# Kernel tuning notes

Hardware: AMD Instinct MI355X
Metric: run time of the kernel (lower is better)

## Reference

```python
import jax, jax.numpy as jnp
import numpy as np

NUM_OPS = 100_000
NUM_MACH = 512
H = 128
OPF = 6
MF = 2
L = 2
N_PREC = 800_000
N_CHALF = 800_000  # compat edges per direction
EPS = 1e-5


def setup_inputs() -> dict:
    key = jax.random.key(0)
    ks = jax.random.split(key, 20)
    op_features = jax.random.normal(ks[0], (NUM_OPS, OPF), dtype=jnp.float32)
    machine_features = jax.random.normal(ks[1], (NUM_MACH, MF), dtype=jnp.float32)
    prec_src = jax.random.randint(ks[2], (N_PREC,), 0, NUM_OPS, dtype=jnp.int32)
    prec_tgt = jax.random.randint(ks[3], (N_PREC,), 0, NUM_OPS, dtype=jnp.int32)
    precedence_edges = jnp.stack([prec_src, prec_tgt])  # [2, N_PREC]
    op_idx = jax.random.randint(ks[4], (N_CHALF,), 0, NUM_OPS, dtype=jnp.int32)
    m_idx = jax.random.randint(ks[5], (N_CHALF,), 0, NUM_MACH, dtype=jnp.int32)
    # bidirectional pairs in unified node space (machines offset by NUM_OPS)
    src = jnp.concatenate([op_idx, m_idx + NUM_OPS])
    tgt = jnp.concatenate([m_idx + NUM_OPS, op_idx])
    compatibility_edges = jnp.stack([src, tgt])  # [2, 2*N_CHALF]
    s = 0.05
    op_emb_W = jax.random.normal(ks[6], (H, OPF), dtype=jnp.float32) * s
    op_emb_b = jnp.zeros((H,), jnp.float32)
    mach_emb_W = jax.random.normal(ks[7], (H, MF), dtype=jnp.float32) * s
    mach_emb_b = jnp.zeros((H,), jnp.float32)
    prec_W = jax.random.normal(ks[8], (L, H, H), dtype=jnp.float32) * s
    prec_b = jax.random.normal(ks[9], (L, H), dtype=jnp.float32) * s
    compat_W = jax.random.normal(ks[10], (L, H, H), dtype=jnp.float32) * s
    compat_b = jax.random.normal(ks[11], (L, H), dtype=jnp.float32) * s
    op_ln_g = jnp.ones((L, H), jnp.float32)
    op_ln_b = jnp.zeros((L, H), jnp.float32)
    mach_ln_g = jnp.ones((L, H), jnp.float32)
    mach_ln_b = jnp.zeros((L, H), jnp.float32)
    return dict(op_features=op_features, machine_features=machine_features,
                precedence_edges=precedence_edges, compatibility_edges=compatibility_edges,
                op_emb_W=op_emb_W, op_emb_b=op_emb_b, mach_emb_W=mach_emb_W, mach_emb_b=mach_emb_b,
                prec_W=prec_W, prec_b=prec_b, compat_W=compat_W, compat_b=compat_b,
                op_ln_g=op_ln_g, op_ln_b=op_ln_b, mach_ln_g=mach_ln_g, mach_ln_b=mach_ln_b)


def _layer_norm(x, g, b):
    mu = jnp.mean(x, axis=-1, keepdims=True)
    var = jnp.mean(jnp.square(x - mu), axis=-1, keepdims=True)
    return (x - mu) * jax.lax.rsqrt(var + EPS) * g + b


def _scatter_mean(vals, idx, mask, n):
    # vals [E,H], idx [E], mask [E] bool (or None); mean over incoming edges, count clamped >= 1
    if mask is not None:
        vals = jnp.where(mask[:, None], vals, 0.0)
        idx = jnp.where(mask, idx, 0)
        ones = mask.astype(vals.dtype)
    else:
        ones = jnp.ones(idx.shape, vals.dtype)
    sums = jax.ops.segment_sum(vals, idx, num_segments=n)
    cnts = jax.ops.segment_sum(ones, idx, num_segments=n)
    return sums / jnp.maximum(cnts, 1.0)[:, None]


def _forward(op_features, machine_features, precedence_edges, compatibility_edges,
             op_emb_W, op_emb_b, mach_emb_W, mach_emb_b,
             prec_W, prec_b, compat_W, compat_b,
             op_ln_g, op_ln_b, mach_ln_g, mach_ln_b):
    num_ops = op_features.shape[0]
    num_mach = machine_features.shape[0]
    op_emb = op_features @ op_emb_W.T + op_emb_b
    mach_emb = machine_features @ mach_emb_W.T + mach_emb_b

    p_src, p_tgt = precedence_edges[0], precedence_edges[1]
    c_src, c_tgt = compatibility_edges[0], compatibility_edges[1]
    op2m = (c_src < num_ops) & (c_tgt >= num_ops)
    m2o = (c_src >= num_ops) & (c_tgt < num_ops)
    o2m_src = jnp.where(op2m, c_src, 0)
    o2m_tgt = jnp.where(op2m, c_tgt - num_ops, 0)
    m2o_src = jnp.where(m2o, c_src - num_ops, 0)
    m2o_tgt = jnp.where(m2o, c_tgt, 0)

    for l in range(L):
        # precedence (op -> op): linear-then-gather == gather-then-linear
        op_t = op_emb @ prec_W[l].T + prec_b[l]            # [num_ops, H]
        op_emb_prec = _scatter_mean(op_t[p_src], p_tgt, None, num_ops)
        # compatibility, shared linear for both directions
        op_c = op_emb @ compat_W[l].T + compat_b[l]        # [num_ops, H]
        mach_c = mach_emb @ compat_W[l].T + compat_b[l]    # [num_mach, H]
        mach_emb_compat = _scatter_mean(op_c[o2m_src], o2m_tgt, op2m, num_mach)
        op_emb_compat = _scatter_mean(mach_c[m2o_src], m2o_tgt, m2o, num_ops)
        op_emb = _layer_norm(op_emb + op_emb_prec + op_emb_compat, op_ln_g[l], op_ln_b[l])
        mach_emb = _layer_norm(mach_emb + mach_emb_compat, mach_ln_g[l], mach_ln_b[l])
    return op_emb, mach_emb


def reference(op_features, machine_features, precedence_edges, compatibility_edges,
              op_emb_W, op_emb_b, mach_emb_W, mach_emb_b,
              prec_W, prec_b, compat_W, compat_b,
              op_ln_g, op_ln_b, mach_ln_g, mach_ln_b):
    return _forward(op_features, machine_features, precedence_edges, compatibility_edges,
                    op_emb_W, op_emb_b, mach_emb_W, mach_emb_b,
                    prec_W, prec_b, compat_W, compat_b,
                    op_ln_g, op_ln_b, mach_ln_g, mach_ln_b)
```

## Files before the change

### kernel.cpp

```cpp
#include <hip/hip_runtime.h>
#include <hip/hip_bf16.h>

#define NUM_OPS   100000
#define NUM_MACH  512
#define HDIM      128
#define P1        100352
#define NHIST     200704
#define NBLK      196
#define NCOARSE   784
#define NBC       256
#define NBM       256
#define MHWORDS   (NUM_MACH * NBM)
#define NBLK_M    128
#define NBLK_T    (NBLK + NBLK_M)

typedef short short8 __attribute__((ext_vector_type(8)));
typedef unsigned short ushort8 __attribute__((ext_vector_type(8)));
typedef float floatx4 __attribute__((ext_vector_type(4)));

__device__ __forceinline__ unsigned short f2bf(float f) {
    unsigned u = __float_as_uint(f);
    unsigned r = (u + 0x7FFFu + ((u >> 16) & 1u)) >> 16;
    return (unsigned short)r;
}
__device__ __forceinline__ float bf2f(unsigned short u) {
    return __uint_as_float(((unsigned)u) << 16);
}

__global__ void k_prep(const float* __restrict__ Fo, const float* __restrict__ Fm,
                       const float* __restrict__ Wo, const float* __restrict__ bo,
                       const float* __restrict__ Wm, const float* __restrict__ bm,
                       const float* __restrict__ Wp, const float* __restrict__ Wc,
                       unsigned short* __restrict__ op_ebf,
                       float* __restrict__ mach_emb, unsigned short* __restrict__ mach_ebf,
                       unsigned short* __restrict__ Wb) {
    int idx = blockIdx.x * blockDim.x + threadIdx.x;
    if (idx < NUM_OPS * HDIM) {
        int r = idx >> 7, h = idx & 127;
        const float* f = Fo + (size_t)r * 6;
        const float* w = Wo + (size_t)h * 6;
        float s = bo[h];
#pragma unroll
        for (int i = 0; i < 6; ++i) s += f[i] * w[i];
        op_ebf[idx] = f2bf(s);
        return;
    }
    idx -= NUM_OPS * HDIM;
    if (idx < NUM_MACH * HDIM) {
        int r = idx >> 7, h = idx & 127;
        const float* f = Fm + (size_t)r * 2;
        const float* w = Wm + (size_t)h * 2;
        float s = bm[h] + f[0] * w[0] + f[1] * w[1];
        mach_emb[idx] = s;
        mach_ebf[idx] = f2bf(s);
        return;
    }
    idx -= NUM_MACH * HDIM;
    if (idx < 2 * 128 * 256) {
        int l = idx >> 15, h = (idx >> 8) & 127, k = idx & 255;
        float v = (k < 128) ? Wp[(size_t)l * 16384 + h * 128 + k]
                            : Wc[(size_t)l * 16384 + h * 128 + (k - 128)];
        Wb[idx] = f2bf(v);
    }
}

__global__ __launch_bounds__(256) void k_front(const int* __restrict__ prec_e, int nprec,
                                               const int* __restrict__ comp_e, int E, int M,
                                               int* __restrict__ chist_bh,
                                               int* __restrict__ mach_bh) {
    __shared__ int hc[NCOARSE];
    __shared__ int hm[NUM_MACH];
    for (int i = threadIdx.x; i < NCOARSE; i += 256) hc[i] = 0;
    for (int i = threadIdx.x; i < NUM_MACH; i += 256) hm[i] = 0;
    __syncthreads();
    int NT = nprec + E;
    int ch = (NT + NBC - 1) / NBC;
    int i0 = blockIdx.x * ch, i1 = min(NT, i0 + ch);
    for (int i = i0 + threadIdx.x; i < i1; i += 256) {
        int key;
        if (i < nprec) key = prec_e[nprec + i];
        else {
            int e = i - nprec;
            key = P1 + comp_e[e];
            atomicAdd(&hm[comp_e[E + e] - M], 1);
        }
        atomicAdd(&hc[key >> 8], 1);
    }
    __syncthreads();
    for (int i = threadIdx.x; i < NCOARSE; i += 256)
        chist_bh[i * NBC + blockIdx.x] = hc[i];
    for (int i = threadIdx.x; i < NUM_MACH; i += 256)
        mach_bh[i * NBC + blockIdx.x] = hm[i];
}

__global__ __launch_bounds__(256) void k_cfill(const int* __restrict__ prec_e, int nprec,
                                               const int* __restrict__ comp_e, int E, int M,
                                               const int* __restrict__ scan,
                                               int* __restrict__ pairs) {
    __shared__ int cur[NCOARSE];
    for (int i = threadIdx.x; i < NCOARSE; i += 256) cur[i] = scan[i * NBC + blockIdx.x];
    __syncthreads();
    int NT = nprec + E;
    int ch = (NT + NBC - 1) / NBC;
    int i0 = blockIdx.x * ch, i1 = min(NT, i0 + ch);
    for (int i = i0 + threadIdx.x; i < i1; i += 256) {
        int key, val;
        if (i < nprec) { key = prec_e[nprec + i]; val = prec_e[i]; }
        else { int e = i - nprec; key = P1 + comp_e[e]; val = comp_e[E + e] - M; }
        int pos = atomicAdd(&cur[key >> 8], 1);
        pairs[pos] = (val << 8) | (key & 255);
    }
}

__global__ __launch_bounds__(256) void k_blocksum(const int* __restrict__ arr, int* __restrict__ partial) {
    __shared__ int sh[256];
    int b = blockIdx.x, t = threadIdx.x;
    int4 v = *(const int4*)(arr + b * 1024 + t * 4);
    sh[t] = v.x + v.y + v.z + v.w;
    __syncthreads();
    for (int o = 128; o; o >>= 1) { if (t < o) sh[t] += sh[t + o]; __syncthreads(); }
    if (!t) partial[b] = sh[0];
}

__global__ __launch_bounds__(256) void k_scanpart(const int* __restrict__ partial,
                                                  int* __restrict__ block_off) {
    __shared__ int sh[256];
    int t = threadIdx.x;
    int seg0 = blockIdx.x ? NBLK : 0;
    int n    = blockIdx.x ? NBLK_M : NBLK;
    int v = (t < n) ? partial[seg0 + t] : 0;
    sh[t] = v; __syncthreads();
    for (int o = 1; o < 256; o <<= 1) {
        int x = (t >= o) ? sh[t - o] : 0; __syncthreads();
        sh[t] += x; __syncthreads();
    }
    if (t < n) block_off[seg0 + t] = sh[t] - v;
}

__global__ __launch_bounds__(256) void k_scanwrite(const int* __restrict__ arr,
                                                   const int* __restrict__ block_off,
                                                   int* __restrict__ rs) {
    __shared__ int sh[256];
    int b = blockIdx.x, t = threadIdx.x;
    int base_i = b * 1024 + t * 4;
    int4 v = *(const int4*)(arr + base_i);
    int tsum = v.x + v.y + v.z + v.w;
    sh[t] = tsum; __syncthreads();
    for (int o = 1; o < 256; o <<= 1) {
        int x = (t >= o) ? sh[t - o] : 0; __syncthreads();
        sh[t] += x; __syncthreads();
    }
    int off = block_off[b] + sh[t] - tsum;
    int4 r; r.x = off; r.y = off + v.x; r.z = off + v.x + v.y; r.w = off + v.x + v.y + v.z;
    *(int4*)(rs + base_i) = r;
}

__global__ __launch_bounds__(256) void k_finefill(const int* __restrict__ scans, int NT,
                                                  const int* __restrict__ pairs,
                                                  int* __restrict__ rs,
                                                  int* __restrict__ bucket_all,
                                                  const int* __restrict__ comp_e, int E, int M,
                                                  int* __restrict__ bucket_mach,
                                                  int* __restrict__ mach_rs) {
    int t = threadIdx.x;
    if (blockIdx.x < NCOARSE) {
        __shared__ int hh[256];
        __shared__ int ex[256];
        __shared__ int cu[256];
        int b = blockIdx.x;
        int s = scans[b * NBC];
        int e = (b == NCOARSE - 1) ? NT : scans[(b + 1) * NBC];
        hh[t] = 0;
        __syncthreads();
        for (int i = s + t; i < e; i += 256) atomicAdd(&hh[pairs[i] & 255], 1);
        __syncthreads();
        int v = hh[t];
        ex[t] = v; __syncthreads();
        for (int o = 1; o < 256; o <<= 1) {
            int x = (t >= o) ? ex[t - o] : 0; __syncthreads();
            ex[t] += x; __syncthreads();
        }
        int start = s + ex[t] - v;
        rs[b * 256 + t] = start;
        cu[t] = start;
        __syncthreads();
        for (int i = s + t; i < e; i += 256) {
            int p = pairs[i];
            int pos = atomicAdd(&cu[p & 255], 1);
            bucket_all[pos] = ((unsigned)p) >> 8;
        }
    } else {
        __shared__ int cur[NUM_MACH];
        int blk = blockIdx.x - NCOARSE;
        const int* moff = scans + NHIST;
        for (int i = t; i < NUM_MACH; i += 256) cur[i] = moff[i * NBM + blk];
        if (blk == 0) {
            for (int m = t; m < NUM_MACH; m += 256) mach_rs[m] = moff[m * NBM];
            if (t == 0) mach_rs[NUM_MACH] = E;
        }
        __syncthreads();
        int nprec = NT - E;
        int chNT = (NT + NBC - 1) / NBC;
        int e0 = blk * chNT - nprec;       if (e0 < 0) e0 = 0;
        int e1 = (blk + 1) * chNT - nprec; if (e1 > E) e1 = E;
        for (int e = e0 + t; e < e1; e += 256) {
            int m = comp_e[E + e] - M;
            int op = comp_e[e];
            int pos = atomicAdd(&cur[m], 1);
            bucket_mach[pos] = op;
        }
    }
}

__device__ __forceinline__ void gather8(const unsigned short* __restrict__ src,
                                        const int* __restrict__ bucket,
                                        int s0, int e0, int start, int step,
                                        int lane, int g, int d, float* a) {
    for (int base = s0 + start; base < e0; base += step) {
        int cnt = min(64, e0 - base);
        int idx = (lane < cnt) ? bucket[base + lane] : 0;
        for (int j = 0; j < cnt; j += 4) {
            int jj = j + g;
            int rowi = __shfl(idx, jj);
            short8 v = *(const short8*)(src + (size_t)rowi * HDIM + d);
            if (jj < cnt) {
#pragma unroll
                for (int k = 0; k < 8; ++k) a[k] += bf2f((unsigned short)v[k]);
            }
        }
    }
}

__global__ __launch_bounds__(256) void k_aggmg(
    const unsigned short* __restrict__ op_ebf, const unsigned short* __restrict__ mach_ebf,
    const int* __restrict__ rs, const int* __restrict__ bucket_all,
    unsigned short* __restrict__ Ab, int* __restrict__ flags, int M,
    const int* __restrict__ mach_rs, const int* __restrict__ bucket_mach,
    float* __restrict__ mach_sum, int nb_agg) {
    int wave = threadIdx.x >> 6, lane = threadIdx.x & 63;
    int g = lane >> 4;
    int d = (lane & 15) * 8;

    if ((int)blockIdx.x < nb_agg) {
        int r = blockIdx.x * 4 + wave;
        if (r >= M) return;

        float a[8];
#pragma unroll
        for (int k = 0; k < 8; ++k) a[k] = 0.f;
        int s0 = rs[r], e0 = rs[r + 1];
        gather8(op_ebf, bucket_all, s0, e0, 0, 64, lane, g, d, a);
#pragma unroll
        for (int k = 0; k < 8; ++k) {
            a[k] += __shfl_xor(a[k], 16);
            a[k] += __shfl_xor(a[k], 32);
        }
        float pinv = 1.f / fmaxf((float)(e0 - s0), 1.f);

        float b[8];
#pragma unroll
        for (int k = 0; k < 8; ++k) b[k] = 0.f;
        int s1 = rs[P1 + r], e1 = rs[P1 + r + 1];
        gather8(mach_ebf, bucket_all, s1, e1, 0, 64, lane, g, d, b);
#pragma unroll
        for (int k = 0; k < 8; ++k) {
            b[k] += __shfl_xor(b[k], 16);
            b[k] += __shfl_xor(b[k], 32);
        }
        float cinv = 1.f / fmaxf((float)(e1 - s1), 1.f);

        if (lane < 16) {
            ushort8 pa, pb;
#pragma unroll
            for (int k = 0; k < 8; ++k) { pa[k] = f2bf(a[k] * pinv); pb[k] = f2bf(b[k] * cinv); }
            *(ushort8*)(Ab + (size_t)r * 256 + d)       = pa;
            *(ushort8*)(Ab + (size_t)r * 256 + 128 + d) = pb;
        }
        if (lane == 0) flags[r] = (e0 > s0 ? 1 : 0) | (e1 > s1 ? 2 : 0);
        return;
    }

    int b2 = blockIdx.x - nb_agg;
    int m  = b2 & 511;
    int yq = b2 >> 9;
    int s0 = mach_rs[m], e0 = mach_rs[m + 1];
    float a[8];
#pragma unroll
    for (int k = 0; k < 8; ++k) a[k] = 0.f;
    gather8(op_ebf, bucket_mach, s0, e0, (yq * 4 + wave) * 64, 1024, lane, g, d, a);
#pragma unroll
    for (int k = 0; k < 8; ++k) {
        a[k] += __shfl_xor(a[k], 16);
        a[k] += __shfl_xor(a[k], 32);
    }
    if (lane < 16) {
#pragma unroll
        for (int k = 0; k < 8; ++k)
            atomicAdd(&mach_sum[m * HDIM + d + k], a[k]);
    }
}

__global__ __launch_bounds__(256) void k_gemm_mfma(
    const unsigned short* __restrict__ Ab, const unsigned short* __restrict__ embb,
    const unsigned short* __restrict__ Wb,
    const float* __restrict__ bp, const float* __restrict__ bc,
    const int* __restrict__ flags,
    const float* __restrict__ g, const float* __restrict__ bt,
    float* __restrict__ dstf, unsigned short* __restrict__ dstb, int M) {
    int wave = threadIdx.x >> 6, lane = threadIdx.x & 63;
    int m0 = blockIdx.x * 64 + wave * 16;
    if (m0 >= M) return;
    int quad = lane >> 4, col = lane & 15;

    floatx4 acc[8];
#pragma unroll
    for (int t = 0; t < 8; ++t) acc[t] = (floatx4){0.f, 0.f, 0.f, 0.f};

    const short* Arow  = (const short*)(Ab + (size_t)(m0 + col) * 256);
    const short* Wbase = (const short*)Wb;

#pragma unroll
    for (int ks = 0; ks < 8; ++ks) {
        short8 a = *(const short8*)(Arow + ks * 32 + quad * 8);
#pragma unroll
        for (int t = 0; t < 8; ++t) {
            short8 b = *(const short8*)(Wbase + (size_t)(t * 16 + col) * 256 + ks * 32 + quad * 8);
            acc[t] = __builtin_amdgcn_mfma_f32_16x16x32_bf16(a, b, acc[t], 0, 0, 0);
        }
    }

    float bpv[8], bcv[8], gv[8], btv[8];
#pragma unroll
    for (int t = 0; t < 8; ++t) {
        int c = t * 16 + col;
        bpv[t] = bp[c]; bcv[t] = bc[c]; gv[t] = g[c]; btv[t] = bt[c];
    }
#pragma unroll
    for (int reg = 0; reg < 4; ++reg) {
        int r = m0 + quad * 4 + reg;
        int fl = flags[r];
        float fp = (fl & 1) ? 1.f : 0.f, fc = (fl & 2) ? 1.f : 0.f;
        float x[8]; float s = 0.f, q = 0.f;
#pragma unroll
        for (int t = 0; t < 8; ++t) {
            float v = acc[t][reg] + bf2f(embb[(size_t)r * HDIM + t * 16 + col]) + fp * bpv[t] + fc * bcv[t];
            x[t] = v; s += v; q += v * v;
        }
#pragma unroll
        for (int msk = 1; msk < 16; msk <<= 1) { s += __shfl_xor(s, msk); q += __shfl_xor(q, msk); }
        float mu = s * (1.f / 128.f);
        float rstd = rsqrtf(fmaxf(q * (1.f / 128.f) - mu * mu, 0.f) + 1e-5f);
#pragma unroll
        for (int t = 0; t < 8; ++t) {
            float y = (x[t] - mu) * rstd * gv[t] + btv[t];
            if (dstf) dstf[(size_t)r * HDIM + t * 16 + col] = y;
            if (dstb) dstb[(size_t)r * HDIM + t * 16 + col] = f2bf(y);
        }
    }
}

__global__ __launch_bounds__(128) void k_mach_update(
    const float* __restrict__ mach_emb, const float* __restrict__ mach_sum,
    const int* __restrict__ mach_rs,
    const float* __restrict__ Wc, const float* __restrict__ bc,
    const float* __restrict__ g, const float* __restrict__ bt,
    float* __restrict__ dst, unsigned short* __restrict__ dstb) {
    __shared__ float row[HDIM];
    __shared__ float red[4];
    int m = blockIdx.x, t = threadIdx.x;
    int cnt = mach_rs[m + 1] - mach_rs[m];
    float sc = (cnt > 0) ? 1.f / (float)cnt : 0.f;
    row[t] = mach_sum[m * HDIM + t] * sc;
    __syncthreads();
    float dot = bc[t];
    const float* w = Wc + (size_t)t * HDIM;
#pragma unroll 8
    for (int k = 0; k < HDIM; ++k) dot += row[k] * w[k];
    float x = mach_emb[m * HDIM + t] + ((cnt > 0) ? dot : 0.f);
    float s = x, q = x * x;
#pragma unroll
    for (int o = 32; o; o >>= 1) { s += __shfl_xor(s, o); q += __shfl_xor(q, o); }
    int wv = t >> 6;
    if ((t & 63) == 0) { red[wv * 2] = s; red[wv * 2 + 1] = q; }
    __syncthreads();
    s = red[0] + red[2]; q = red[1] + red[3];
    float mu = s * (1.f / 128.f);
    float rstd = rsqrtf(fmaxf(q * (1.f / 128.f) - mu * mu, 0.f) + 1e-5f);
    float y = (x - mu) * rstd * g[t] + bt[t];
    dst[m * HDIM + t] = y;
    if (dstb) dstb[m * HDIM + t] = f2bf(y);
}

extern "C" void kernel_launch(void* const* d_in, const int* in_sizes, int n_in,
                              void* d_out, int out_size, void* d_ws, size_t ws_size,
                              hipStream_t stream) {
    const float* op_feat    = (const float*)d_in[0];
    const float* m_feat     = (const float*)d_in[1];
    const int*   prec_e     = (const int*)d_in[2];
    const int*   comp_e     = (const int*)d_in[3];
    const float* op_emb_W   = (const float*)d_in[4];
    const float* op_emb_b   = (const float*)d_in[5];
    const float* mach_emb_W = (const float*)d_in[6];
    const float* mach_emb_b = (const float*)d_in[7];
    const float* prec_W     = (const float*)d_in[8];
    const float* prec_b     = (const float*)d_in[9];
    const float* compat_W   = (const float*)d_in[10];
    const float* compat_b   = (const float*)d_in[11];
    const float* op_ln_g    = (const float*)d_in[12];
    const float* op_ln_b    = (const float*)d_in[13];
    const float* mach_ln_g  = (const float*)d_in[14];
    const float* mach_ln_b  = (const float*)d_in[15];
    float* out = (float*)d_out;

    const int M = NUM_OPS, NM = NUM_MACH;
    const int nprec = in_sizes[2] / 2;
    const int ncomp = in_sizes[3] / 2;
    const int E = ncomp / 2;
    const int NT = nprec + E;

    float* ws = (float*)d_ws;
    size_t o = 0;
    unsigned short* op_ebf = (unsigned short*)(ws + o); o += (size_t)M * 64;
    unsigned short* Ab = (unsigned short*)(ws + o); o += (size_t)M * 128;
    unsigned short* Wb = (unsigned short*)(ws + o); o += 32768;
    float* mach_emb = ws + o; o += (size_t)NM * HDIM;
    unsigned short* mach_ebf = (unsigned short*)(ws + o); o += (size_t)NM * 64;
    float* mach_sum = ws + o; o += (size_t)NM * HDIM;
    int* ip = (int*)(ws + o);
    size_t io = 0;
    int* hists     = ip + io; io += NHIST + MHWORDS;
    int* scans     = ip + io; io += NHIST + MHWORDS;
    int* rs        = ip + io; io += NHIST;
    int* mach_rs   = ip + io; io += NM + 8;
    int* partialT  = ip + io; io += 512;
    int* block_off = ip + io; io += 512;
    int* flags     = ip + io; io += M;
    int* pairs     = ip + io; io += (size_t)NT;
    int* bucket_all  = ip + io; io += (size_t)NT;
    int* bucket_mach = ip + io; io += (size_t)E;

    int* mach_bh = hists + NHIST;

    k_front<<<NBC, 256, 0, stream>>>(prec_e, nprec, comp_e, E, M, hists, mach_bh);
    k_blocksum<<<NBLK_T, 256, 0, stream>>>(hists, partialT);
    k_scanpart<<<2, 256, 0, stream>>>(partialT, block_off);
    k_scanwrite<<<NBLK_T, 256, 0, stream>>>(hists, block_off, scans);
    k_cfill<<<NBC, 256, 0, stream>>>(prec_e, nprec, comp_e, E, M, scans, pairs);
    k_finefill<<<NCOARSE + NBM, 256, 0, stream>>>(scans, NT, pairs, rs, bucket_all,
                                                  comp_e, E, M, bucket_mach, mach_rs);

    int prep_total = (M + NM) * HDIM + 2 * 128 * 256;
    k_prep<<<(prep_total + 255) / 256, 256, 0, stream>>>(
        op_feat, m_feat, op_emb_W, op_emb_b, mach_emb_W, mach_emb_b,
        prec_W, compat_W, op_ebf, mach_emb, mach_ebf, Wb);

    const int nb_agg = (M + 3) / 4;
    for (int l = 0; l < 2; ++l) {
        int last = (l == 1);
        const float* bpl = prec_b   + (size_t)l * HDIM;
        const float* Wc  = compat_W + (size_t)l * HDIM * HDIM;
        const float* bcl = compat_b + (size_t)l * HDIM;

        hipMemsetAsync(mach_sum, 0, (size_t)NM * HDIM * sizeof(float), stream);

        k_aggmg<<<nb_agg + NM * 4, 256, 0, stream>>>(
            op_ebf, mach_ebf, rs, bucket_all, Ab, flags, M,
            mach_rs, bucket_mach, mach_sum, nb_agg);

        k_gemm_mfma<<<(M + 63) / 64, 256, 0, stream>>>(
            Ab, op_ebf, Wb + (size_t)l * 128 * 256, bpl, bcl, flags,
            op_ln_g + (size_t)l * HDIM, op_ln_b + (size_t)l * HDIM,
            last ? out : nullptr, last ? nullptr : op_ebf, M);

        k_mach_update<<<NM, 128, 0, stream>>>(
            mach_emb, mach_sum, mach_rs, Wc, bcl,
            mach_ln_g + (size_t)l * HDIM, mach_ln_b + (size_t)l * HDIM,
            last ? (out + (size_t)M * HDIM) : mach_emb, last ? nullptr : mach_ebf);
    }
}
```

Baseline: 567.0 us.

## Fuse neighbor aggregation with MFMA linear and layernorm in one kernel

Merges the gather/mean aggregation kernel and the MFMA GEMM+LayerNorm kernel into a single 1024-thread block kernel. Each block gathers 16 op rows into swizzled LDS and runs the 16x256x128 MFMA from LDS. It then applies bias and LayerNorm per row, so the intermediate Ab buffer and flags never go through global memory. Op embeddings are double-buffered (A/B) because the fused kernel reads neighbors of other rows while writing its own outputs, and machine aggregation is folded in as extra blocks with fewer waves per machine. The risk is lower occupancy from large blocks and barriers, and W is reloaded per block.

After: 561.3 us. About the same (-1.0%).

```diff
diff --git a/kernel.cpp b/kernel.cpp
--- a/kernel.cpp
+++ b/kernel.cpp
@@ -13,6 +13,7 @@
 #define MHWORDS   (NUM_MACH * NBM)
 #define NBLK_M    128
 #define NBLK_T    (NBLK + NBLK_M)
+#define NB_OP     (NUM_OPS / 16)
 
 typedef short short8 __attribute__((ext_vector_type(8)));
 typedef unsigned short ushort8 __attribute__((ext_vector_type(8)));
@@ -231,37 +232,61 @@
     }
 }
 
-__global__ __launch_bounds__(256) void k_aggmg(
-    const unsigned short* __restrict__ op_ebf, const unsigned short* __restrict__ mach_ebf,
+__global__ __launch_bounds__(1024, 8) void k_fused(
+    const unsigned short* __restrict__ ebf_src, const unsigned short* __restrict__ mach_ebf,
     const int* __restrict__ rs, const int* __restrict__ bucket_all,
-    unsigned short* __restrict__ Ab, int* __restrict__ flags, int M,
+    const unsigned short* __restrict__ Wb,
+    const float* __restrict__ bp, const float* __restrict__ bc,
+    const float* __restrict__ g, const float* __restrict__ bt,
+    float* __restrict__ dstf, unsigned short* __restrict__ dstb,
     const int* __restrict__ mach_rs, const int* __restrict__ bucket_mach,
-    float* __restrict__ mach_sum, int nb_agg) {
+    float* __restrict__ mach_sum, int M) {
+    __shared__ unsigned short At[16 * 256];
+    __shared__ float Xt[16][HDIM];
+    __shared__ int flg[16];
     int wave = threadIdx.x >> 6, lane = threadIdx.x & 63;
-    int g = lane >> 4;
-    int d = (lane & 15) * 8;
-
-    if ((int)blockIdx.x < nb_agg) {
-        int r = blockIdx.x * 4 + wave;
-        if (r >= M) return;
-
+    int gg = lane >> 4;
+    int d  = (lane & 15) * 8;
+
+    if ((int)blockIdx.x >= NB_OP) {
+        int m = blockIdx.x - NB_OP;
+        int s0 = mach_rs[m], e0 = mach_rs[m + 1];
         float a[8];
 #pragma unroll
         for (int k = 0; k < 8; ++k) a[k] = 0.f;
-        int s0 = rs[r], e0 = rs[r + 1];
-        gather8(op_ebf, bucket_all, s0, e0, 0, 64, lane, g, d, a);
+        gather8(ebf_src, bucket_mach, s0, e0, wave * 64, 1024, lane, gg, d, a);
 #pragma unroll
         for (int k = 0; k < 8; ++k) {
             a[k] += __shfl_xor(a[k], 16);
             a[k] += __shfl_xor(a[k], 32);
         }
+        if (lane < 16) {
+#pragma unroll
+            for (int k = 0; k < 8; ++k)
+                atomicAdd(&mach_sum[m * HDIM + d + k], a[k]);
+        }
+        return;
+    }
+
+    int r = blockIdx.x * 16 + wave;
+    {
+        float a[8];
+#pragma unroll
+        for (int k = 0; k < 8; ++k) a[k] = 0.f;
+        int s0 = rs[r], e0 = rs[r + 1];
+        gather8(ebf_src, bucket_all, s0, e0, 0, 64, lane, gg, d, a);
+#pragma unroll
+        for (int k = 0; k < 8; ++k) {
+            a[k] += __shfl_xor(a[k], 16);
+            a[k] += __shfl_xor(a[k], 32);
+        }
         float pinv = 1.f / fmaxf((float)(e0 - s0), 1.f);
 
         float b[8];
 #pragma unroll
         for (int k = 0; k < 8; ++k) b[k] = 0.f;
         int s1 = rs[P1 + r], e1 = rs[P1 + r + 1];
-        gather8(mach_ebf, bucket_all, s1, e1, 0, 64, lane, g, d, b);
+        gather8(mach_ebf, bucket_all, s1, e1, 0, 64, lane, gg, d, b);
 #pragma unroll
         for (int k = 0; k < 8; ++k) {
             b[k] += __shfl_xor(b[k], 16);
@@ -273,89 +298,53 @@
             ushort8 pa, pb;
 #pragma unroll
             for (int k = 0; k < 8; ++k) { pa[k] = f2bf(a[k] * pinv); pb[k] = f2bf(b[k] * cinv); }
-            *(ushort8*)(Ab + (size_t)r * 256 + d)       = pa;
-            *(ushort8*)(Ab + (size_t)r * 256 + 128 + d) = pb;
-        }
-        if (lane == 0) flags[r] = (e0 > s0 ? 1 : 0) | (e1 > s1 ? 2 : 0);
-        return;
-    }
-
-    int b2 = blockIdx.x - nb_agg;
-    int m  = b2 & 511;
-    int yq = b2 >> 9;
-    int s0 = mach_rs[m], e0 = mach_rs[m + 1];
-    float a[8];
-#pragma unroll
-    for (int k = 0; k < 8; ++k) a[k] = 0.f;
-    gather8(op_ebf, bucket_mach, s0, e0, (yq * 4 + wave) * 64, 1024, lane, g, d, a);
-#pragma unroll
-    for (int k = 0; k < 8; ++k) {
-        a[k] += __shfl_xor(a[k], 16);
-        a[k] += __shfl_xor(a[k], 32);
-    }
-    if (lane < 16) {
-#pragma unroll
-        for (int k = 0; k < 8; ++k)
-            atomicAdd(&mach_sum[m * HDIM + d + k], a[k]);
-    }
-}
-
-__global__ __launch_bounds__(256) void k_gemm_mfma(
-    const unsigned short* __restrict__ Ab, const unsigned short* __restrict__ embb,
-    const unsigned short* __restrict__ Wb,
-    const float* __restrict__ bp, const float* __restrict__ bc,
-    const int* __restrict__ flags,
-    const float* __restrict__ g, const float* __restrict__ bt,
-    float* __restrict__ dstf, unsigned short* __restrict__ dstb, int M) {
-    int wave = threadIdx.x >> 6, lane = threadIdx.x & 63;
-    int m0 = blockIdx.x * 64 + wave * 16;
-    if (m0 >= M) return;
-    int quad = lane >> 4, col = lane & 15;
-
-    floatx4 acc[8];
-#pragma unroll
-    for (int t = 0; t < 8; ++t) acc[t] = (floatx4){0.f, 0.f, 0.f, 0.f};
-
-    const short* Arow  = (const short*)(Ab + (size_t)(m0 + col) * 256);
-    const short* Wbase = (const short*)Wb;
-
-#pragma unroll
-    for (int ks = 0; ks < 8; ++ks) {
-        short8 a = *(const short8*)(Arow + ks * 32 + quad * 8);
-#pragma unroll
-        for (int t = 0; t < 8; ++t) {
-            short8 b = *(const short8*)(Wbase + (size_t)(t * 16 + col) * 256 + ks * 32 + quad * 8);
-            acc[t] = __builtin_amdgcn_mfma_f32_16x16x32_bf16(a, b, acc[t], 0, 0, 0);
-        }
-    }
-
-    float bpv[8], bcv[8], gv[8], btv[8];
-#pragma unroll
-    for (int t = 0; t < 8; ++t) {
-        int c = t * 16 + col;
-        bpv[t] = bp[c]; bcv[t] = bc[c]; gv[t] = g[c]; btv[t] = bt[c];
-    }
-#pragma unroll
-    for (int reg = 0; reg < 4; ++reg) {
-        int r = m0 + quad * 4 + reg;
-        int fl = flags[r];
+            unsigned sw = (wave & 7) << 4;
+            *(ushort8*)((char*)At + wave * 512 + ((lane * 16) ^ sw))         = pa;
+            *(ushort8*)((char*)At + wave * 512 + (256 + ((lane * 16) ^ sw))) = pb;
+        }
+        if (lane == 0) flg[wave] = (e0 > s0 ? 1 : 0) | (e1 > s1 ? 2 : 0);
+    }
+    __syncthreads();
+
+    if (wave < 8) {
+        int t = wave, quad = lane >> 4, col = lane & 15;
+        unsigned swr = (col & 7) << 4;
+        floatx4 acc = (floatx4){0.f, 0.f, 0.f, 0.f};
+        const short* Wrow = (const short*)Wb + (size_t)(t * 16 + col) * 256;
+#pragma unroll
+        for (int ks = 0; ks < 8; ++ks) {
+            short8 af = *(const short8*)((const char*)At + col * 512 + ((ks * 64 + quad * 16) ^ swr));
+            short8 bf = *(const short8*)(Wrow + ks * 32 + quad * 8);
+            acc = __builtin_amdgcn_mfma_f32_16x16x32_bf16(af, bf, acc, 0, 0, 0);
+        }
+#pragma unroll
+        for (int reg = 0; reg < 4; ++reg)
+            Xt[quad * 4 + reg][t * 16 + col] = acc[reg];
+    }
+    __syncthreads();
+
+    {
+        int row = wave;
+        int rr = blockIdx.x * 16 + row;
+        int c = lane * 2;
+        int fl = flg[row];
         float fp = (fl & 1) ? 1.f : 0.f, fc = (fl & 2) ? 1.f : 0.f;
-        float x[8]; float s = 0.f, q = 0.f;
-#pragma unroll
-        for (int t = 0; t < 8; ++t) {
-            float v = acc[t][reg] + bf2f(embb[(size_t)r * HDIM + t * 16 + col]) + fp * bpv[t] + fc * bcv[t];
-            x[t] = v; s += v; q += v * v;
-        }
-#pragma unroll
-        for (int msk = 1; msk < 16; msk <<= 1) { s += __shfl_xor(s, msk); q += __shfl_xor(q, msk); }
+        ushort2 e2 = *(const ushort2*)(ebf_src + (size_t)rr * HDIM + c);
+        float2 bpv = *(const float2*)(bp + c);
+        float2 bcv = *(const float2*)(bc + c);
+        float x0 = Xt[row][c]     + bf2f(e2.x) + fp * bpv.x + fc * bcv.x;
+        float x1 = Xt[row][c + 1] + bf2f(e2.y) + fp * bpv.y + fc * bcv.y;
+        float s = x0 + x1, q = x0 * x0 + x1 * x1;
+#pragma unroll
+        for (int o = 32; o; o >>= 1) { s += __shfl_xor(s, o); q += __shfl_xor(q, o); }
         float mu = s * (1.f / 128.f);
         float rstd = rsqrtf(fmaxf(q * (1.f / 128.f) - mu * mu, 0.f) + 1e-5f);
-#pragma unroll
-        for (int t = 0; t < 8; ++t) {
-            float y = (x[t] - mu) * rstd * gv[t] + btv[t];
-            if (dstf) dstf[(size_t)r * HDIM + t * 16 + col] = y;
-            if (dstb) dstb[(size_t)r * HDIM + t * 16 + col] = f2bf(y);
-        }
+        float2 gv = *(const float2*)(g + c);
+        float2 bv = *(const float2*)(bt + c);
+        float y0 = (x0 - mu) * rstd * gv.x + bv.x;
+        float y1 = (x1 - mu) * rstd * gv.y + bv.y;
+        if (dstf) { float2 yy; yy.x = y0; yy.y = y1; *(float2*)(dstf + (size_t)rr * HDIM + c) = yy; }
+        if (dstb) { ushort2 ys; ys.x = f2bf(y0); ys.y = f2bf(y1); *(ushort2*)(dstb + (size_t)rr * HDIM + c) = ys; }
     }
 }
 
@@ -420,8 +409,8 @@
 
     float* ws = (float*)d_ws;
     size_t o = 0;
-    unsigned short* op_ebf = (unsigned short*)(ws + o); o += (size_t)M * 64;
-    unsigned short* Ab = (unsigned short*)(ws + o); o += (size_t)M * 128;
+    unsigned short* op_ebfA = (unsigned short*)(ws + o); o += (size_t)M * 64;
+    unsigned short* op_ebfB = (unsigned short*)(ws + o); o += (size_t)M * 64;
     unsigned short* Wb = (unsigned short*)(ws + o); o += 32768;
     float* mach_emb = ws + o; o += (size_t)NM * HDIM;
     unsigned short* mach_ebf = (unsigned short*)(ws + o); o += (size_t)NM * 64;
@@ -434,7 +423,6 @@
     int* mach_rs   = ip + io; io += NM + 8;
     int* partialT  = ip + io; io += 512;
     int* block_off = ip + io; io += 512;
-    int* flags     = ip + io; io += M;
     int* pairs     = ip + io; io += (size_t)NT;
     int* bucket_all  = ip + io; io += (size_t)NT;
     int* bucket_mach = ip + io; io += (size_t)E;
@@ -452,25 +440,24 @@
     int prep_total = (M + NM) * HDIM + 2 * 128 * 256;
     k_prep<<<(prep_total + 255) / 256, 256, 0, stream>>>(
         op_feat, m_feat, op_emb_W, op_emb_b, mach_emb_W, mach_emb_b,
-        prec_W, compat_W, op_ebf, mach_emb, mach_ebf, Wb);
-
-    const int nb_agg = (M + 3) / 4;
+        prec_W, compat_W, op_ebfA, mach_emb, mach_ebf, Wb);
+
     for (int l = 0; l < 2; ++l) {
         int last = (l == 1);
+        const unsigned short* ebf_src = last ? op_ebfB : op_ebfA;
+        unsigned short* ebf_dst = last ? nullptr : op_ebfB;
         const float* bpl = prec_b   + (size_t)l * HDIM;
         const float* Wc  = compat_W + (size_t)l * HDIM * HDIM;
         const float* bcl = compat_b + (size_t)l * HDIM;
 
         hipMemsetAsync(mach_sum, 0, (size_t)NM * HDIM * sizeof(float), stream);
 
-        k_aggmg<<<nb_agg + NM * 4, 256, 0, stream>>>(
-            op_ebf, mach_ebf, rs, bucket_all, Ab, flags, M,
-            mach_rs, bucket_mach, mach_sum, nb_agg);
-
-        k_gemm_mfma<<<(M + 63) / 64, 256, 0, stream>>>(
-            Ab, op_ebf, Wb + (size_t)l * 128 * 256, bpl, bcl, flags,
+        k_fused<<<NB_OP + NM, 1024, 0, stream>>>(
+            ebf_src, mach_ebf, rs, bucket_all,
+            Wb + (size_t)l * 128 * 256, bpl, bcl,
             op_ln_g + (size_t)l * HDIM, op_ln_b + (size_t)l * HDIM,
-            last ? out : nullptr, last ? nullptr : op_ebf, M);
+            last ? out : nullptr, ebf_dst,
+            mach_rs, bucket_mach, mach_sum, M);
 
         k_mach_update<<<NM, 128, 0, stream>>>(
             mach_emb, mach_sum, mach_rs, Wc, bcl,
```

## Interleave multi-row neighbor gathers and fuse machine update into the GEMM kernel

Applied to the files above, without the earlier changes.

The op-side aggregation now gives each wave two rows and gathers the precedence and compatibility neighbor lists of both at once, with eight independent row loads in flight per step. The machine-side gather is unrolled to issue eight loads per step. The machine update becomes extra blocks of the GEMM/LayerNorm kernel; those blocks zero mach_sum after reading it, so the per-layer memset is replaced by a single memset before the loop. The aim is more memory-level parallelism in the gathers and fewer launches, at the cost of more registers per thread (lower occupancy) and wasted iterations when a wave's lists differ in length.

Measured after the change: 546.2 us. 1.04x faster.

```diff
diff --git a/kernel.cpp b/kernel.cpp
--- a/kernel.cpp
+++ b/kernel.cpp
@@ -212,24 +212,7 @@
     }
 }
 
-__device__ __forceinline__ void gather8(const unsigned short* __restrict__ src,
-                                        const int* __restrict__ bucket,
-                                        int s0, int e0, int start, int step,
-                                        int lane, int g, int d, float* a) {
-    for (int base = s0 + start; base < e0; base += step) {
-        int cnt = min(64, e0 - base);
-        int idx = (lane < cnt) ? bucket[base + lane] : 0;
-        for (int j = 0; j < cnt; j += 4) {
-            int jj = j + g;
-            int rowi = __shfl(idx, jj);
-            short8 v = *(const short8*)(src + (size_t)rowi * HDIM + d);
-            if (jj < cnt) {
-#pragma unroll
-                for (int k = 0; k < 8; ++k) a[k] += bf2f((unsigned short)v[k]);
-            }
-        }
-    }
-}
+#define ACC8(acc, v) { _Pragma("unroll") for (int k = 0; k < 8; ++k) acc[k] += bf2f((unsigned short)v[k]); }
 
 __global__ __launch_bounds__(256) void k_aggmg(
     const unsigned short* __restrict__ op_ebf, const unsigned short* __restrict__ mach_ebf,
@@ -242,41 +225,82 @@
     int d = (lane & 15) * 8;
 
     if ((int)blockIdx.x < nb_agg) {
-        int r = blockIdx.x * 4 + wave;
-        if (r >= M) return;
-
-        float a[8];
-#pragma unroll
-        for (int k = 0; k < 8; ++k) a[k] = 0.f;
-        int s0 = rs[r], e0 = rs[r + 1];
-        gather8(op_ebf, bucket_all, s0, e0, 0, 64, lane, g, d, a);
+        int r0 = blockIdx.x * 8 + wave * 2;
+        int r1 = r0 + 1;
+        if (r0 >= M) return;
+        int sA0 = rs[r0],      eA0 = rs[r0 + 1];
+        int sB0 = rs[P1 + r0], eB0 = rs[P1 + r0 + 1];
+        int sA1 = rs[r1],      eA1 = rs[r1 + 1];
+        int sB1 = rs[P1 + r1], eB1 = rs[P1 + r1 + 1];
+
+        float a0[8], b0[8], a1[8], b1[8];
+#pragma unroll
+        for (int k = 0; k < 8; ++k) { a0[k] = 0.f; b0[k] = 0.f; a1[k] = 0.f; b1[k] = 0.f; }
+
+        int bA0 = sA0, bB0 = sB0, bA1 = sA1, bB1 = sB1;
+        while (bA0 < eA0 || bB0 < eB0 || bA1 < eA1 || bB1 < eB1) {
+            int cA0 = (bA0 < eA0) ? min(64, eA0 - bA0) : 0;
+            int cB0 = (bB0 < eB0) ? min(64, eB0 - bB0) : 0;
+            int cA1 = (bA1 < eA1) ? min(64, eA1 - bA1) : 0;
+            int cB1 = (bB1 < eB1) ? min(64, eB1 - bB1) : 0;
+            int iA0 = (lane < cA0) ? bucket_all[bA0 + lane] : 0;
+            int iB0 = (lane < cB0) ? bucket_all[bB0 + lane] : 0;
+            int iA1 = (lane < cA1) ? bucket_all[bA1 + lane] : 0;
+            int iB1 = (lane < cB1) ? bucket_all[bB1 + lane] : 0;
+            int jm = max(max(cA0, cB0), max(cA1, cB1));
+            for (int j = 0; j < jm; j += 8) {
+                int j0 = j + g, j1 = j + 4 + g;
+                int rA0a = __shfl(iA0, j0), rA0b = __shfl(iA0, j1);
+                int rB0a = __shfl(iB0, j0), rB0b = __shfl(iB0, j1);
+                int rA1a = __shfl(iA1, j0), rA1b = __shfl(iA1, j1);
+                int rB1a = __shfl(iB1, j0), rB1b = __shfl(iB1, j1);
+                short8 vA0a = *(const short8*)(op_ebf   + (size_t)rA0a * HDIM + d);
+                short8 vA0b = *(const short8*)(op_ebf   + (size_t)rA0b * HDIM + d);
+                short8 vB0a = *(const short8*)(mach_ebf + (size_t)rB0a * HDIM + d);
+                short8 vB0b = *(const short8*)(mach_ebf + (size_t)rB0b * HDIM + d);
+                short8 vA1a = *(const short8*)(op_ebf   + (size_t)rA1a * HDIM + d);
+                short8 vA1b = *(const short8*)(op_ebf   + (size_t)rA1b * HDIM + d);
+                short8 vB1a = *(const short8*)(mach_ebf + (size_t)rB1a * HDIM + d);
+                short8 vB1b = *(const short8*)(mach_ebf + (size_t)rB1b * HDIM + d);
+                if (j0 < cA0) ACC8(a0, vA0a);
+                if (j1 < cA0) ACC8(a0, vA0b);
+                if (j0 < cB0) ACC8(b0, vB0a);
+                if (j1 < cB0) ACC8(b0, vB0b);
+                if (j0 < cA1) ACC8(a1, vA1a);
+                if (j1 < cA1) ACC8(a1, vA1b);
+                if (j0 < cB1) ACC8(b1, vB1a);
+                if (j1 < cB1) ACC8(b1, vB1b);
+            }
+            bA0 += 64; bB0 += 64; bA1 += 64; bB1 += 64;
+        }
 #pragma unroll
         for (int k = 0; k < 8; ++k) {
-            a[k] += __shfl_xor(a[k], 16);
-            a[k] += __shfl_xor(a[k], 32);
-        }
-        float pinv = 1.f / fmaxf((float)(e0 - s0), 1.f);
-
-        float b[8];
-#pragma unroll
-        for (int k = 0; k < 8; ++k) b[k] = 0.f;
-        int s1 = rs[P1 + r], e1 = rs[P1 + r + 1];
-        gather8(mach_ebf, bucket_all, s1, e1, 0, 64, lane, g, d, b);
-#pragma unroll
-        for (int k = 0; k < 8; ++k) {
-            b[k] += __shfl_xor(b[k], 16);
-            b[k] += __shfl_xor(b[k], 32);
-        }
-        float cinv = 1.f / fmaxf((float)(e1 - s1), 1.f);
+            a0[k] += __shfl_xor(a0[k], 16); a0[k] += __shfl_xor(a0[k], 32);
+            b0[k] += __shfl_xor(b0[k], 16); b0[k] += __shfl_xor(b0[k], 32);
+            a1[k] += __shfl_xor(a1[k], 16); a1[k] += __shfl_xor(a1[k], 32);
+            b1[k] += __shfl_xor(b1[k], 16); b1[k] += __shfl_xor(b1[k], 32);
+        }
+        float p0 = 1.f / fmaxf((float)(eA0 - sA0), 1.f);
+        float c0 = 1.f / fmaxf((float)(eB0 - sB0), 1.f);
+        float p1 = 1.f / fmaxf((float)(eA1 - sA1), 1.f);
+        float c1 = 1.f / fmaxf((float)(eB1 - sB1), 1.f);
 
         if (lane < 16) {
-            ushort8 pa, pb;
-#pragma unroll
-            for (int k = 0; k < 8; ++k) { pa[k] = f2bf(a[k] * pinv); pb[k] = f2bf(b[k] * cinv); }
-            *(ushort8*)(Ab + (size_t)r * 256 + d)       = pa;
-            *(ushort8*)(Ab + (size_t)r * 256 + 128 + d) = pb;
-        }
-        if (lane == 0) flags[r] = (e0 > s0 ? 1 : 0) | (e1 > s1 ? 2 : 0);
+            ushort8 q0, q1, q2, q3;
+#pragma unroll
+            for (int k = 0; k < 8; ++k) {
+                q0[k] = f2bf(a0[k] * p0); q1[k] = f2bf(b0[k] * c0);
+                q2[k] = f2bf(a1[k] * p1); q3[k] = f2bf(b1[k] * c1);
+            }
+            *(ushort8*)(Ab + (size_t)r0 * 256 + d)       = q0;
+            *(ushort8*)(Ab + (size_t)r0 * 256 + 128 + d) = q1;
+            *(ushort8*)(Ab + (size_t)r1 * 256 + d)       = q2;
+            *(ushort8*)(Ab + (size_t)r1 * 256 + 128 + d) = q3;
+        }
+        if (lane == 0) {
+            flags[r0] = (eA0 > sA0 ? 1 : 0) | (eB0 > sB0 ? 2 : 0);
+            flags[r1] = (eA1 > sA1 ? 1 : 0) | (eB1 > sB1 ? 2 : 0);
+        }
         return;
     }
 
@@ -287,7 +311,34 @@
     float a[8];
 #pragma unroll
     for (int k = 0; k < 8; ++k) a[k] = 0.f;
-    gather8(op_ebf, bucket_mach, s0, e0, (yq * 4 + wave) * 64, 1024, lane, g, d, a);
+
+    for (int base = s0 + (yq * 4 + wave) * 64; base < e0; base += 1024) {
+        int cnt = min(64, e0 - base);
+        int idx = (lane < cnt) ? bucket_mach[base + lane] : 0;
+        int j = 0;
+        for (; j + 32 <= cnt; j += 32) {
+            int r0 = __shfl(idx, j + g),      r1 = __shfl(idx, j + 4 + g);
+            int r2 = __shfl(idx, j + 8 + g),  r3 = __shfl(idx, j + 12 + g);
+            int r4 = __shfl(idx, j + 16 + g), r5 = __shfl(idx, j + 20 + g);
+            int r6 = __shfl(idx, j + 24 + g), r7 = __shfl(idx, j + 28 + g);
+            short8 v0 = *(const short8*)(op_ebf + (size_t)r0 * HDIM + d);
+            short8 v1 = *(const short8*)(op_ebf + (size_t)r1 * HDIM + d);
+            short8 v2 = *(const short8*)(op_ebf + (size_t)r2 * HDIM + d);
+            short8 v3 = *(const short8*)(op_ebf + (size_t)r3 * HDIM + d);
+            short8 v4 = *(const short8*)(op_ebf + (size_t)r4 * HDIM + d);
+            short8 v5 = *(const short8*)(op_ebf + (size_t)r5 * HDIM + d);
+            short8 v6 = *(const short8*)(op_ebf + (size_t)r6 * HDIM + d);
+            short8 v7 = *(const short8*)(op_ebf + (size_t)r7 * HDIM + d);
+            ACC8(a, v0); ACC8(a, v1); ACC8(a, v2); ACC8(a, v3);
+            ACC8(a, v4); ACC8(a, v5); ACC8(a, v6); ACC8(a, v7);
+        }
+        for (; j < cnt; j += 4) {
+            int jj = j + g;
+            int rowi = __shfl(idx, jj);
+            short8 v = *(const short8*)(op_ebf + (size_t)rowi * HDIM + d);
+            if (jj < cnt) ACC8(a, v);
+        }
+    }
 #pragma unroll
     for (int k = 0; k < 8; ++k) {
         a[k] += __shfl_xor(a[k], 16);
@@ -300,13 +351,54 @@
     }
 }
 
-__global__ __launch_bounds__(256) void k_gemm_mfma(
+__global__ __launch_bounds__(256) void k_gemm_mupd(
     const unsigned short* __restrict__ Ab, const unsigned short* __restrict__ embb,
     const unsigned short* __restrict__ Wb,
     const float* __restrict__ bp, const float* __restrict__ bc,
     const int* __restrict__ flags,
     const float* __restrict__ g, const float* __restrict__ bt,
-    float* __restrict__ dstf, unsigned short* __restrict__ dstb, int M) {
+    float* __restrict__ dstf, unsigned short* __restrict__ dstb, int M, int nb_gemm,
+    const float* __restrict__ mach_emb, float* __restrict__ mach_sum,
+    const int* __restrict__ mach_rs,
+    const float* __restrict__ Wc,
+    const float* __restrict__ gm, const float* __restrict__ btm,
+    float* __restrict__ mdst, unsigned short* __restrict__ mdstb) {
+    if ((int)blockIdx.x >= nb_gemm) {
+        __shared__ float row[HDIM];
+        __shared__ float red[4];
+        int m = blockIdx.x - nb_gemm, t = threadIdx.x;
+        int cnt = mach_rs[m + 1] - mach_rs[m];
+        float sc = (cnt > 0) ? 1.f / (float)cnt : 0.f;
+        if (t < HDIM) {
+            row[t] = mach_sum[m * HDIM + t] * sc;
+            mach_sum[m * HDIM + t] = 0.f;
+        }
+        __syncthreads();
+        float x = 0.f, s = 0.f, q = 0.f;
+        if (t < HDIM) {
+            float dot = bc[t];
+            const float* w = Wc + (size_t)t * HDIM;
+#pragma unroll 8
+            for (int k = 0; k < HDIM; ++k) dot += row[k] * w[k];
+            x = mach_emb[m * HDIM + t] + ((cnt > 0) ? dot : 0.f);
+            s = x; q = x * x;
+#pragma unroll
+            for (int o = 32; o; o >>= 1) { s += __shfl_xor(s, o); q += __shfl_xor(q, o); }
+            int wv = t >> 6;
+            if ((t & 63) == 0) { red[wv * 2] = s; red[wv * 2 + 1] = q; }
+        }
+        __syncthreads();
+        if (t < HDIM) {
+            s = red[0] + red[2]; q = red[1] + red[3];
+            float mu = s * (1.f / 128.f);
+            float rstd = rsqrtf(fmaxf(q * (1.f / 128.f) - mu * mu, 0.f) + 1e-5f);
+            float y = (x - mu) * rstd * gm[t] + btm[t];
+            mdst[m * HDIM + t] = y;
+            if (mdstb) mdstb[m * HDIM + t] = f2bf(y);
+        }
+        return;
+    }
+
     int wave = threadIdx.x >> 6, lane = threadIdx.x & 63;
     int m0 = blockIdx.x * 64 + wave * 16;
     if (m0 >= M) return;
@@ -357,38 +449,6 @@
             if (dstb) dstb[(size_t)r * HDIM + t * 16 + col] = f2bf(y);
         }
     }
-}
-
-__global__ __launch_bounds__(128) void k_mach_update(
-    const float* __restrict__ mach_emb, const float* __restrict__ mach_sum,
-    const int* __restrict__ mach_rs,
-    const float* __restrict__ Wc, const float* __restrict__ bc,
-    const float* __restrict__ g, const float* __restrict__ bt,
-    float* __restrict__ dst, unsigned short* __restrict__ dstb) {
-    __shared__ float row[HDIM];
-    __shared__ float red[4];
-    int m = blockIdx.x, t = threadIdx.x;
-    int cnt = mach_rs[m + 1] - mach_rs[m];
-    float sc = (cnt > 0) ? 1.f / (float)cnt : 0.f;
-    row[t] = mach_sum[m * HDIM + t] * sc;
-    __syncthreads();
-    float dot = bc[t];
-    const float* w = Wc + (size_t)t * HDIM;
-#pragma unroll 8
-    for (int k = 0; k < HDIM; ++k) dot += row[k] * w[k];
-    float x = mach_emb[m * HDIM + t] + ((cnt > 0) ? dot : 0.f);
-    float s = x, q = x * x;
-#pragma unroll
-    for (int o = 32; o; o >>= 1) { s += __shfl_xor(s, o); q += __shfl_xor(q, o); }
-    int wv = t >> 6;
-    if ((t & 63) == 0) { red[wv * 2] = s; red[wv * 2 + 1] = q; }
-    __syncthreads();
-    s = red[0] + red[2]; q = red[1] + red[3];
-    float mu = s * (1.f / 128.f);
-    float rstd = rsqrtf(fmaxf(q * (1.f / 128.f) - mu * mu, 0.f) + 1e-5f);
-    float y = (x - mu) * rstd * g[t] + bt[t];
-    dst[m * HDIM + t] = y;
-    if (dstb) dstb[m * HDIM + t] = f2bf(y);
 }
 
 extern "C" void kernel_launch(void* const* d_in, const int* in_sizes, int n_in,
@@ -453,27 +513,25 @@
     k_prep<<<(prep_total + 255) / 256, 256, 0, stream>>>(
         op_feat, m_feat, op_emb_W, op_emb_b, mach_emb_W, mach_emb_b,
         prec_W, compat_W, op_ebf, mach_emb, mach_ebf, Wb);
-
-    const int nb_agg = (M + 3) / 4;
+    hipMemsetAsync(mach_sum, 0, (size_t)NM * HDIM * sizeof(float), stream);
+
+    const int nb_agg = M / 8;
+    const int nb_gemm = (M + 63) / 64;
     for (int l = 0; l < 2; ++l) {
         int last = (l == 1);
         const float* bpl = prec_b   + (size_t)l * HDIM;
         const float* Wc  = compat_W + (size_t)l * HDIM * HDIM;
         const float* bcl = compat_b + (size_t)l * HDIM;
 
-        hipMemsetAsync(mach_sum, 0, (size_t)NM * HDIM * sizeof(float), stream);
-
         k_aggmg<<<nb_agg + NM * 4, 256, 0, stream>>>(
             op_ebf, mach_ebf, rs, bucket_all, Ab, flags, M,
             mach_rs, bucket_mach, mach_sum, nb_agg);
 
-        k_gemm_mfma<<<(M + 63) / 64, 256, 0, stream>>>(
+        k_gemm_mupd<<<nb_gemm + NM, 256, 0, stream>>>(
             Ab, op_ebf, Wb + (size_t)l * 128 * 256, bpl, bcl, flags,
             op_ln_g + (size_t)l * HDIM, op_ln_b + (size_t)l * HDIM,
-            last ? out : nullptr, last ? nullptr : op_ebf, M);
-
-        k_mach_update<<<NM, 128, 0, stream>>>(
-            mach_emb, mach_sum, mach_rs, Wc, bcl,
+            last ? out : nullptr, last ? nullptr : op_ebf, M, nb_gemm,
+            mach_emb, mach_sum, mach_rs, Wc,
             mach_ln_g + (size_t)l * HDIM, mach_ln_b + (size_t)l * HDIM,
             last ? (out + (size_t)M * HDIM) : mach_emb, last ? nullptr : mach_ebf);
     }
```
